# Kernel optimization log

Measured on AMD Instinct MI355X. Metric: run time of the kernel, lower is better.

Reference implementation:

```python
import jax, jax.numpy as jnp
import numpy as np
from jax import lax

A_RATIOS = (0.5, 1.0, 2.0)
A_SCALES = (8, 16, 32)
FEAT_STRIDE = 16
BASE_SIZE = 16
PRE_NMS = 6000     # n_test_pre_nms
POST_NMS = 300     # n_test_post_nms
NMS_THRESH = 0.7
MIN_SIZE = 16.0
SCALE = 1.0        # forward(scale=1.0) default
NEG = -1e10


def _anchor_base():
    # standard generate_anchor_base: centered at (8,8), ratios x scales
    py = px = BASE_SIZE / 2.0
    rows = []
    for r in A_RATIOS:
        for s in A_SCALES:
            h = BASE_SIZE * s * np.sqrt(r)
            w = BASE_SIZE * s * np.sqrt(1.0 / r)
            rows.append([py - h / 2.0, px - w / 2.0, py + h / 2.0, px + w / 2.0])
    return np.asarray(rows, np.float32)  # (A, 4)


def _all_anchors(height, width):
    base = jnp.asarray(_anchor_base())                                  # (A, 4)
    sy = (jnp.arange(height) * FEAT_STRIDE).astype(jnp.float32)
    sx = (jnp.arange(width) * FEAT_STRIDE).astype(jnp.float32)
    gy, gx = jnp.meshgrid(sy, sx, indexing='ij')
    shift = jnp.stack([gy.ravel(), gx.ravel(), gy.ravel(), gx.ravel()], axis=1)  # (K, 4)
    anch = base[None, :, :] + shift[:, None, :]                         # (K, A, 4)
    return anch.reshape(-1, 4)                                          # (K*A, 4)


def _conv(x, w, b, pad):
    y = lax.conv_general_dilated(x, w, (1, 1), [(pad, pad), (pad, pad)],
                                 dimension_numbers=('NCHW', 'OIHW', 'NCHW'))
    return y + b[None, :, None, None]


def _loc2bbox(anchors, locs):
    h = anchors[:, 2] - anchors[:, 0]
    w = anchors[:, 3] - anchors[:, 1]
    cy = anchors[:, 0] + 0.5 * h
    cx = anchors[:, 1] + 0.5 * w
    dy, dx, dh, dw = locs[:, 0], locs[:, 1], locs[:, 2], locs[:, 3]
    ncy = dy * h + cy
    ncx = dx * w + cx
    nh = jnp.exp(dh) * h
    nw = jnp.exp(dw) * w
    return jnp.stack([ncy - 0.5 * nh, ncx - 0.5 * nw,
                      ncy + 0.5 * nh, ncx + 0.5 * nw], axis=1)


def _iou_one_vs_all(box, boxes):
    ty = jnp.maximum(box[0], boxes[:, 0])
    tx = jnp.maximum(box[1], boxes[:, 1])
    by = jnp.minimum(box[2], boxes[:, 2])
    bx = jnp.minimum(box[3], boxes[:, 3])
    inter = jnp.maximum(by - ty, 0.0) * jnp.maximum(bx - tx, 0.0)
    a1 = (box[2] - box[0]) * (box[3] - box[1])
    a2 = (boxes[:, 2] - boxes[:, 0]) * (boxes[:, 3] - boxes[:, 1])
    return inter / (a1 + a2 - inter + 1e-9)


def _nms(boxes, scores):
    # greedy NMS with fixed POST_NMS output; invalid slots are zero boxes
    def step(s, _):
        i = jnp.argmax(s)
        valid = s[i] > NEG / 2
        ious = _iou_one_vs_all(boxes[i], boxes)
        s = jnp.where(ious > NMS_THRESH, NEG, s)  # suppresses self (iou=1)
        return s, (i, valid)
    _, (idx, valid) = lax.scan(step, scores, None, length=POST_NMS)
    return boxes[idx] * valid[:, None].astype(boxes.dtype)  # (POST_NMS, 4)


def _proposals(anchors, locs, fg, img_h, img_w):
    boxes = _loc2bbox(anchors, locs)
    boxes = jnp.stack([jnp.clip(boxes[:, 0], 0.0, img_h),
                       jnp.clip(boxes[:, 1], 0.0, img_w),
                       jnp.clip(boxes[:, 2], 0.0, img_h),
                       jnp.clip(boxes[:, 3], 0.0, img_w)], axis=1)
    hs = boxes[:, 2] - boxes[:, 0]
    ws = boxes[:, 3] - boxes[:, 1]
    ok = (hs >= MIN_SIZE * SCALE) & (ws >= MIN_SIZE * SCALE)
    sc = jnp.where(ok, fg, NEG)
    top_sc, idx = lax.top_k(sc, PRE_NMS)
    return _nms(boxes[idx], top_sc)


def reference(base_feat, W_conv1, b_conv1, W_score, b_score, W_loc, b_loc, img_h, img_w):
    N, _, H, W = base_feat.shape
    A = 9
    mid = jax.nn.relu(_conv(base_feat, W_conv1, b_conv1, 1))            # (N,512,H,W)
    rpn_locs = _conv(mid, W_loc, b_loc, 0).transpose(0, 2, 3, 1).reshape(N, H * W * A, 4)
    raw = _conv(mid, W_score, b_score, 0).transpose(0, 2, 3, 1)          # (N,H,W,2A)
    rpn_scores = raw.reshape(N, H * W * A, 2)
    fg = jax.nn.softmax(raw.reshape(N, H, W, A, 2), axis=-1)[..., 1].reshape(N, -1)
    anchors = _all_anchors(H, W)                                         # (H*W*A,4)
    ih, iw = float(img_h), float(img_w)
    prop = jax.vmap(lambda l, f: _proposals(anchors, l, f, ih, iw))(rpn_locs, fg)
    rois = prop.reshape(N * POST_NMS, 4)
    roi_indices = jnp.repeat(jnp.arange(N, dtype=jnp.int32), POST_NMS)
    return rpn_locs, rpn_scores, rois, roi_indices, anchors


def setup_inputs() -> dict:
    key = jax.random.key(0)
    k0, k1, k2, k3 = jax.random.split(key, 4)
    N, C, H, W = 4, 512, 64, 64
    nA = 9
    return {
        'base_feat': jax.random.normal(k0, (N, C, H, W), jnp.float32),
        'W_conv1': 0.01 * jax.random.normal(k1, (512, 512, 3, 3), jnp.float32),
        'b_conv1': jnp.zeros((512,), jnp.float32),
        'W_score': 0.01 * jax.random.normal(k2, (2 * nA, 512, 1, 1), jnp.float32),
        'b_score': jnp.zeros((2 * nA,), jnp.float32),
        'W_loc': 0.01 * jax.random.normal(k3, (4 * nA, 512, 1, 1), jnp.float32),
        'b_loc': jnp.zeros((4 * nA,), jnp.float32),
        'img_h': 1024,
        'img_w': 1024,
    }
```

## Files before the change

### kernel.cpp

```cpp
#include <hip/hip_runtime.h>
#include <math.h>

#define HH 64
#define WW 64
#define NIMG 4
#define CIN 512
#define AA 9
#define HWA (HH*WW*AA)
#define PRE_NMS 6000
#define POST_NMS 300
#define NEGV (-1e10f)
#define NEGK 0xD01502F9u
#define NWORD 94

#define OFF1 589824
#define OFF2 884736
#define OFF3 889536
#define OFF4 890736

typedef unsigned int u32;
typedef unsigned long long u64;
typedef _Float16 f16;
typedef _Float16 half8 __attribute__((ext_vector_type(8)));
typedef float f32x4 __attribute__((ext_vector_type(4)));

struct AnchBase { float v[36]; };

__device__ __forceinline__ void gload_lds16(const void* g, void* l)
{
    __builtin_amdgcn_global_load_lds((const __attribute__((address_space(1))) void*)g,
                                     (__attribute__((address_space(3))) void*)l,
                                     16, 0, 0);
}

__global__ __launch_bounds__(256) void k_prep_x(const float* __restrict__ x,
                                                f16* __restrict__ xh,
                                                f16* __restrict__ xl)
{
    __shared__ float tile[64][65];
    int ci0 = blockIdx.x * 64, y = blockIdx.y, n = blockIdx.z;
    int t = threadIdx.x;
    #pragma unroll
    for (int l = 0; l < 16; ++l) {
        int idx = l * 256 + t;
        int cc = idx >> 6, xc = idx & 63;
        tile[cc][xc] = x[((size_t)(n * CIN + ci0 + cc) * HH + y) * WW + xc];
    }
    __syncthreads();
    #pragma unroll
    for (int l = 0; l < 16; ++l) {
        int idx = l * 256 + t;
        int xc = idx >> 6, cc = idx & 63;
        float v = tile[cc][xc];
        f16 hi = (f16)v;
        f16 lo = (f16)(v - (float)hi);
        size_t o = ((size_t)(n * 64 + y) * 64 + xc) * 512 + ci0 + cc;
        xh[o] = hi; xl[o] = lo;
    }
}

__global__ __launch_bounds__(256) void k_prep_w(const float* __restrict__ W1,
                                                f16* __restrict__ wh,
                                                f16* __restrict__ wl)
{
    int idx = blockIdx.x * 256 + threadIdx.x;
    int co = idx >> 9, ci = idx & 511;
    #pragma unroll
    for (int tap = 0; tap < 9; ++tap) {
        float v = W1[(size_t)idx * 9 + tap];
        f16 hi = (f16)v;
        f16 lo = (f16)(v - (float)hi);
        size_t o = ((size_t)tap * 512 + co) * 512 + ci;
        wh[o] = hi; wl[o] = lo;
    }
}

__global__ __launch_bounds__(256, 4) void k_conv_mfma(const f16* __restrict__ xh,
                                                      const f16* __restrict__ xl,
                                                      const f16* __restrict__ wh,
                                                      const f16* __restrict__ wl,
                                                      const float* __restrict__ bias,
                                                      float* __restrict__ mid)
{
    __shared__ f16 sX[2][4][66][32];
    const int t = threadIdx.x;
    const int lid = blockIdx.x + 8 * (blockIdx.y + 32 * blockIdx.z);
    const int logical = (lid & 7) * 128 + (lid >> 3);
    const int co0 = (logical & 7) * 64;
    const int g = logical >> 3;
    const int yb = g & 31, n = g >> 5;
    const int y0 = yb * 2;
    const int wv = t >> 6, lane = t & 63;
    const int q = lane >> 4, li = lane & 15;
    const int mh = wv & 1;
    const int xhp = wv >> 1;

    {
        int pr = t >> 5, j = t & 31;
        int col = (j < 16) ? 0 : 65, e = j & 15;
        u32* p = (u32*)&sX[0][0][0][0];
        p[(pr >> 2) * 4224 + (pr & 3) * 1056 + col * 16 + e] = 0;
    }
    if (yb == 0 || yb == 31) {
        int r = (yb == 0) ? 0 : 3;
        u32* p = (u32*)&sX[0][0][0][0];
        #pragma unroll
        for (int l = 0; l < 9; ++l) {
            int idx = l * 256 + t;
            if (idx < 2112) {
                int plane = (idx >= 1056) ? 1 : 0;
                int rr = idx - plane * 1056;
                p[plane * 4224 + r * 1056 + rr] = 0;
            }
        }
    }

    f32x4 acc[2][2][2];
    #pragma unroll
    for (int mt = 0; mt < 2; ++mt)
        #pragma unroll
        for (int xn = 0; xn < 2; ++xn)
            #pragma unroll
            for (int yy = 0; yy < 2; ++yy)
                acc[mt][xn][yy] = (f32x4){0.f, 0.f, 0.f, 0.f};

    auto prefetch = [&](int ci0) {
        #pragma unroll
        for (int m = 0; m < 8; ++m) {
            int k2 = wv * 8 + m;
            int plane = k2 >> 4;
            int row = (k2 >> 2) & 3;
            int gy = y0 - 1 + row;
            if ((unsigned)gy < 64u) {
                int col = ((k2 & 3) << 4) + (lane >> 2);
                int s = (lane & 3) ^ ((lane >> 3) & 3);
                const f16* src = (plane ? xl : xh) +
                    (((size_t)(n * 64 + gy) * 64 + col) * 512 + ci0 + s * 8);
                f16* dst = &sX[0][0][0][0] + (size_t)plane * 8448 + row * 2112
                           + (1 + (k2 & 3) * 16) * 32 + lane * 8;
                gload_lds16(src, dst);
            }
        }
    };

    const size_t wb0 = (size_t)(co0 + mh * 32 + li) * 512 + q * 8;
    const f16* pWh = wh + wb0;
    const f16* pWl = wl + wb0;
    half8 wa[2][2], wn[2][2];
    auto loadW = [&](half8 (&w)[2][2], int ci0, int tap) {
        #pragma unroll
        for (int mt = 0; mt < 2; ++mt) {
            size_t off = (size_t)tap * 262144 + (size_t)mt * 8192 + ci0;
            w[0][mt] = *(const half8*)(pWh + off);
            w[1][mt] = *(const half8*)(pWl + off);
        }
    };

    const f16* pB[2][3];
    #pragma unroll
    for (int xn = 0; xn < 2; ++xn)
        #pragma unroll
        for (int kx = 0; kx < 3; ++kx) {
            int lc = xhp * 32 + xn * 16 + li + kx;
            int qe = q ^ (((lc - 1) >> 1) & 3);
            pB[xn][kx] = &sX[0][0][0][0] + lc * 32 + qe * 8;
        }

    auto loadB = [&](half8 (&Bf)[2][2][2], int tap) {
        const int ky = tap / 3, kx = tap - ky * 3;
        #pragma unroll
        for (int xn = 0; xn < 2; ++xn) {
            const f16* pb = pB[xn][kx];
            #pragma unroll
            for (int yy = 0; yy < 2; ++yy) {
                const f16* ph = pb + (yy + ky) * 2112;
                Bf[0][xn][yy] = *(const half8*)ph;
                Bf[1][xn][yy] = *(const half8*)(ph + 8448);
            }
        }
    };

    prefetch(0);
    loadW(wa, 0, 0);

    for (int chunk = 0; chunk < 16; ++chunk) {
        const int ci0 = chunk * 32;
        __syncthreads();

        half8 B0[2][2][2], Bn[2][2][2];
        loadB(B0, 0);

        #pragma unroll
        for (int tap = 0; tap < 9; ++tap) {
            if (tap < 8) {
                loadW(wn, ci0, tap + 1);
                loadB(Bn, tap + 1);
            }
            #pragma unroll
            for (int mt = 0; mt < 2; ++mt)
                #pragma unroll
                for (int xn = 0; xn < 2; ++xn)
                    #pragma unroll
                    for (int yy = 0; yy < 2; ++yy)
                        acc[mt][xn][yy] = __builtin_amdgcn_mfma_f32_16x16x32_f16(wa[0][mt], B0[0][xn][yy], acc[mt][xn][yy], 0, 0, 0);
            #pragma unroll
            for (int mt = 0; mt < 2; ++mt)
                #pragma unroll
                for (int xn = 0; xn < 2; ++xn)
                    #pragma unroll
                    for (int yy = 0; yy < 2; ++yy)
                        acc[mt][xn][yy] = __builtin_amdgcn_mfma_f32_16x16x32_f16(wa[0][mt], B0[1][xn][yy], acc[mt][xn][yy], 0, 0, 0);
            #pragma unroll
            for (int mt = 0; mt < 2; ++mt)
                #pragma unroll
                for (int xn = 0; xn < 2; ++xn)
                    #pragma unroll
                    for (int yy = 0; yy < 2; ++yy)
                        acc[mt][xn][yy] = __builtin_amdgcn_mfma_f32_16x16x32_f16(wa[1][mt], B0[0][xn][yy], acc[mt][xn][yy], 0, 0, 0);

            if (tap < 8) {
                #pragma unroll
                for (int pl = 0; pl < 2; ++pl)
                    #pragma unroll
                    for (int mt = 0; mt < 2; ++mt) wa[pl][mt] = wn[pl][mt];
                #pragma unroll
                for (int pl = 0; pl < 2; ++pl)
                    #pragma unroll
                    for (int xn = 0; xn < 2; ++xn)
                        #pragma unroll
                        for (int yy = 0; yy < 2; ++yy) B0[pl][xn][yy] = Bn[pl][xn][yy];
            }
        }

        if (chunk + 1 < 16) {
            __syncthreads();
            prefetch(ci0 + 32);
            loadW(wa, ci0 + 32, 0);
        }
    }

    #pragma unroll
    for (int mt = 0; mt < 2; ++mt) {
        #pragma unroll
        for (int r = 0; r < 4; ++r) {
            int co = co0 + mh * 32 + mt * 16 + q * 4 + r;
            float bv = bias[co];
            #pragma unroll
            for (int xn = 0; xn < 2; ++xn) {
                int xc = xhp * 32 + xn * 16 + li;
                #pragma unroll
                for (int yy = 0; yy < 2; ++yy) {
                    float v = acc[mt][xn][yy][r] + bv;
                    mid[((size_t)(n * 512 + co) * HH + y0 + yy) * WW + xc] = v > 0.f ? v : 0.f;
                }
            }
        }
    }
}

__global__ __launch_bounds__(256) void k_htrans(const float* __restrict__ Ws,
                                                const float* __restrict__ Wl,
                                                float* __restrict__ Wt2)
{
    int i = blockIdx.x * 256 + threadIdx.x;
    if (i >= 512 * 64) return;
    int ci = i >> 6, co = i & 63;
    float v = 0.f;
    if (co < 18) v = Ws[co * 512 + ci];
    else if (co < 54) v = Wl[(co - 18) * 512 + ci];
    Wt2[i] = v;
}

__global__ __launch_bounds__(256) void k_hgemm(const float* __restrict__ mid,
                                               const float* __restrict__ Wt2,
                                               float* __restrict__ sraw)
{
    __shared__ float sM[32][64];
    __shared__ float sW2[32][64];
    const int t = threadIdx.x;
    const int px0 = blockIdx.x * 64, n = blockIdx.y;
    const int tx = t & 15, ty = t >> 4;

    float acc[4][4];
    #pragma unroll
    for (int c = 0; c < 4; ++c)
        #pragma unroll
        for (int j = 0; j < 4; ++j) acc[c][j] = 0.f;

    for (int ci0 = 0; ci0 < 512; ci0 += 32) {
        __syncthreads();
        #pragma unroll
        for (int l = 0; l < 8; ++l) {
            int i = l * 256 + t;
            int ci = i >> 6, px = i & 63;
            sM[ci][px] = mid[((size_t)n * 512 + ci0 + ci) * 4096 + px0 + px];
            sW2[ci][px] = Wt2[(size_t)(ci0 + ci) * 64 + px];
        }
        __syncthreads();
        #pragma unroll
        for (int ci = 0; ci < 32; ++ci) {
            float mv[4], wv[4];
            #pragma unroll
            for (int j = 0; j < 4; ++j) mv[j] = sM[ci][tx * 4 + j];
            #pragma unroll
            for (int c = 0; c < 4; ++c) wv[c] = sW2[ci][ty * 4 + c];
            #pragma unroll
            for (int c = 0; c < 4; ++c)
                #pragma unroll
                for (int j = 0; j < 4; ++j) acc[c][j] += wv[c] * mv[j];
        }
    }
    #pragma unroll
    for (int c = 0; c < 4; ++c) {
        float4 v = make_float4(acc[c][0], acc[c][1], acc[c][2], acc[c][3]);
        *(float4*)&sraw[((size_t)n * 64 + ty * 4 + c) * 4096 + px0 + tx * 4] = v;
    }
}

__global__ __launch_bounds__(256) void k_decode(const float* __restrict__ sraw,
                                                const float* __restrict__ bsc,
                                                const float* __restrict__ blc,
                                                const int* __restrict__ ph,
                                                const int* __restrict__ pw,
                                                float* __restrict__ out,
                                                float* __restrict__ boxes,
                                                u32* __restrict__ key,
                                                AnchBase ab)
{
    int p = blockIdx.x * 256 + threadIdx.x;
    int n = p >> 12, pi = p & 4095;
    int y = pi >> 6, xq = pi & 63;

    const float* S = sraw + (size_t)n * 64 * 4096 + pi;
    float* o0 = out + (size_t)n * 147456;
    float* o1 = out + OFF1 + (size_t)n * 73728;
    float IHf = (float)(*ph), IWf = (float)(*pw);

    #pragma unroll
    for (int a = 0; a < 9; ++a) {
        float s0 = S[(size_t)(2 * a) * 4096] + bsc[2 * a];
        float s1 = S[(size_t)(2 * a + 1) * 4096] + bsc[2 * a + 1];
        float dy = S[(size_t)(18 + 4 * a) * 4096] + blc[4 * a];
        float dx = S[(size_t)(19 + 4 * a) * 4096] + blc[4 * a + 1];
        float dh = S[(size_t)(20 + 4 * a) * 4096] + blc[4 * a + 2];
        float dw = S[(size_t)(21 + 4 * a) * 4096] + blc[4 * a + 3];

        o1[(pi * 9 + a) * 2 + 0] = s0;
        o1[(pi * 9 + a) * 2 + 1] = s1;
        o0[(pi * 9 + a) * 4 + 0] = dy;
        o0[(pi * 9 + a) * 4 + 1] = dx;
        o0[(pi * 9 + a) * 4 + 2] = dh;
        o0[(pi * 9 + a) * 4 + 3] = dw;

        float mm = fmaxf(s0, s1);
        float e0 = expf(s0 - mm), e1 = expf(s1 - mm);
        float fg = e1 / (e0 + e1);

        float a0 = ab.v[4 * a + 0] + (float)(y * 16);
        float a1 = ab.v[4 * a + 1] + (float)(xq * 16);
        float a2 = ab.v[4 * a + 2] + (float)(y * 16);
        float a3 = ab.v[4 * a + 3] + (float)(xq * 16);

        float h = a2 - a0, w = a3 - a1;
        float cy = a0 + 0.5f * h, cx = a1 + 0.5f * w;
        float ncy = dy * h + cy, ncx = dx * w + cx;
        float nh = expf(dh) * h, nw = expf(dw) * w;
        float b0 = fminf(fmaxf(ncy - 0.5f * nh, 0.f), IHf);
        float b1 = fminf(fmaxf(ncx - 0.5f * nw, 0.f), IWf);
        float b2 = fminf(fmaxf(ncy + 0.5f * nh, 0.f), IHf);
        float b3 = fminf(fmaxf(ncx + 0.5f * nw, 0.f), IWf);

        bool ok = (b2 - b0 >= 16.0f) && (b3 - b1 >= 16.0f);
        float sc = ok ? fg : NEGV;

        int gi = n * HWA + pi * 9 + a;
        ((float4*)boxes)[gi] = make_float4(b0, b1, b2, b3);
        u32 u = __float_as_uint(sc);
        u32 kasc = (u & 0x80000000u) ? ~u : (u | 0x80000000u);
        key[gi] = ~kasc;
    }
}

__global__ void k_misc(float* __restrict__ out, AnchBase ab)
{
    int i = blockIdx.x * 256 + threadIdx.x;
    if (i < 4800) out[OFF2 + i] = 0.f;
    if (i < 1200) out[OFF3 + i] = (float)(i / 300);
    if (i < HWA) {
        int pi = i / 9, a = i - pi * 9;
        int y = pi >> 6, xq = pi & 63;
        out[OFF4 + i * 4 + 0] = ab.v[4 * a + 0] + (float)(y * 16);
        out[OFF4 + i * 4 + 1] = ab.v[4 * a + 1] + (float)(xq * 16);
        out[OFF4 + i * 4 + 2] = ab.v[4 * a + 2] + (float)(y * 16);
        out[OFF4 + i * 4 + 3] = ab.v[4 * a + 3] + (float)(xq * 16);
    }
}

__global__ __launch_bounds__(1024) void k_select(const u32* __restrict__ key,
                                                 u64* __restrict__ cmp,
                                                 int* __restrict__ nvalid)
{
    __shared__ int hist[256];
    __shared__ u32 sPref;
    __shared__ int sR;
    __shared__ int cLess, cEq, cVal;
    int n = blockIdx.x, t = threadIdx.x;
    const u32* k0 = key + (size_t)n * HWA;

    u32 pref = 0, mask = 0;
    int R = PRE_NMS;
    for (int pass = 0; pass < 4; ++pass) {
        int shift = 24 - pass * 8;
        if (t < 256) hist[t] = 0;
        __syncthreads();
        for (int i = t; i < HWA; i += 1024) {
            u32 k = k0[i];
            if ((k & mask) == pref) atomicAdd(&hist[(k >> shift) & 255], 1);
        }
        __syncthreads();
        if (t == 0) {
            int cum = 0;
            for (int b = 0; b < 256; ++b) {
                int c = hist[b];
                if (cum + c >= R) { sPref = pref | ((u32)b << shift); sR = R - cum; break; }
                cum += c;
            }
        }
        __syncthreads();
        pref = sPref; R = sR; mask |= (0xFFu << shift);
        __syncthreads();
    }
    u32 T = pref;
    if (t == 0) { cLess = 0; cEq = 0; cVal = 0; }
    __syncthreads();
    for (int i = t; i < HWA; i += 1024) {
        u32 k = k0[i];
        if (k < NEGK) atomicAdd(&cVal, 1);
        if (k < T) {
            int p = atomicAdd(&cLess, 1);
            cmp[(size_t)n * 8192 + p] = ((u64)k << 32) | (u32)i;
        } else if (k == T) {
            int p = atomicAdd(&cEq, 1);
            if (p < R) cmp[(size_t)n * 8192 + (PRE_NMS - 1 - p)] = ((u64)k << 32) | (u32)i;
        }
    }
    for (int i = PRE_NMS + t; i < 8192; i += 1024) cmp[(size_t)n * 8192 + i] = ~0ull;
    __syncthreads();
    if (t == 0) nvalid[n] = cVal < PRE_NMS ? cVal : PRE_NMS;
}

__global__ __launch_bounds__(1024) void k_sort(const u64* __restrict__ cmp,
                                               const float* __restrict__ boxes,
                                               float* __restrict__ boxesS)
{
    __shared__ u64 sK[8192];
    int n = blockIdx.x, t = threadIdx.x;
    for (int i = t; i < 8192; i += 1024) sK[i] = cmp[(size_t)n * 8192 + i];
    for (unsigned k = 2; k <= 8192; k <<= 1) {
        for (unsigned j = k >> 1; j > 0; j >>= 1) {
            __syncthreads();
            #pragma unroll
            for (int v = 0; v < 8; ++v) {
                int i = v * 1024 + t;
                int ixj = i ^ (int)j;
                if (ixj > i) {
                    u64 a = sK[i], b = sK[ixj];
                    bool up = ((i & (int)k) == 0);
                    if (up ? (a > b) : (a < b)) { sK[i] = b; sK[ixj] = a; }
                }
            }
        }
    }
    __syncthreads();
    const float4* bsrc = (const float4*)boxes + (size_t)n * HWA;
    float4* bdst = (float4*)boxesS + (size_t)n * PRE_NMS;
    for (int i = t; i < PRE_NMS; i += 1024) {
        u32 idx = (u32)(sK[i] & 0xFFFFFFFFu);
        bdst[i] = bsrc[idx];
    }
}

__global__ __launch_bounds__(64) void k_iou(const float* __restrict__ boxesS,
                                            u64* __restrict__ mask)
{
    __shared__ float4 cb[64];
    int w = blockIdx.x, ic = blockIdx.y, n = blockIdx.z;
    if (w < ic) return;
    int t = threadIdx.x;
    const float4* B = (const float4*)boxesS + (size_t)n * PRE_NMS;
    int jc = w * 64 + t;
    cb[t] = (jc < PRE_NMS) ? B[jc] : make_float4(0.f, 0.f, 0.f, 0.f);
    __syncthreads();
    int i = ic * 64 + t;
    if (i >= PRE_NMS) return;
    float4 bb = B[i];
    float area1 = (bb.z - bb.x) * (bb.w - bb.y);
    u64 m = 0;
    #pragma unroll 8
    for (int j = 0; j < 64; ++j) {
        float4 o = cb[j];
        float ty_ = fmaxf(bb.x, o.x), tx_ = fmaxf(bb.y, o.y);
        float by_ = fminf(bb.z, o.z), bx_ = fminf(bb.w, o.w);
        float inter = fmaxf(by_ - ty_, 0.f) * fmaxf(bx_ - tx_, 0.f);
        float area2 = (o.z - o.x) * (o.w - o.y);
        float iou = inter / (area1 + area2 - inter + 1e-9f);
        if (iou > 0.7f) m |= (1ull << j);
    }
    mask[((size_t)n * PRE_NMS + i) * NWORD + w] = m;
}

__global__ __launch_bounds__(64) void k_nms3(const u64* __restrict__ mask,
                                             const int* __restrict__ nvalid,
                                             const float* __restrict__ boxesS,
                                             float* __restrict__ rois)
{
    int n = blockIdx.x, lane = threadIdx.x;
    int nv = nvalid[n];
    const u64* M = mask + (size_t)n * PRE_NMS * NWORD;
    const float4* B = (const float4*)boxesS + (size_t)n * PRE_NMS;

    auto vmask = [&](int w) -> u64 {
        int lo = w * 64;
        if (nv >= lo + 64) return ~0ull;
        if (nv <= lo) return 0ull;
        return (1ull << (nv - lo)) - 1ull;
    };
    u64 vm0 = vmask(lane);
    u64 vm1 = (lane < NWORD - 64) ? vmask(64 + lane) : 0ull;
    u64 rem0 = 0, rem1 = 0;

    int cnt = 0;
    while (cnt < POST_NMS) {
        u64 c0 = (~rem0) & vm0;
        u64 c1 = (~rem1) & vm1;
        int sel;
        u64 b0 = __ballot(c0 != 0);
        if (b0) {
            int l = __builtin_ctzll(b0);
            u64 w = __shfl(c0, l);
            sel = l * 64 + __builtin_ctzll(w);
        } else {
            u64 b1 = __ballot(c1 != 0);
            if (!b1) break;
            int l = __builtin_ctzll(b1);
            u64 w = __shfl(c1, l);
            sel = (64 + l) * 64 + __builtin_ctzll(w);
        }
        if (lane == 0) {
            float4 bb = B[sel];
            float* orow = rois + (size_t)(n * POST_NMS + cnt) * 4;
            orow[0] = bb.x; orow[1] = bb.y; orow[2] = bb.z; orow[3] = bb.w;
        }
        const u64* Mr = M + (size_t)sel * NWORD;
        rem0 |= Mr[lane];
        if (lane < NWORD - 64) rem1 |= Mr[64 + lane];
        cnt++;
    }
}

extern "C" void kernel_launch(void* const* d_in, const int* in_sizes, int n_in,
                              void* d_out, int out_size, void* d_ws, size_t ws_size,
                              hipStream_t stream)
{
    const float* x  = (const float*)d_in[0];
    const float* W1 = (const float*)d_in[1];
    const float* b1 = (const float*)d_in[2];
    const float* Ws = (const float*)d_in[3];
    const float* bs = (const float*)d_in[4];
    const float* Wl = (const float*)d_in[5];
    const float* bl = (const float*)d_in[6];
    const int* ih   = (const int*)d_in[7];
    const int* iw   = (const int*)d_in[8];
    float* out = (float*)d_out;
    char* ws = (char*)d_ws;

    f16*   Wh2    = (f16*)  (ws);
    f16*   Wl2    = (f16*)  (ws + 4718592);
    float* mid    = (float*)(ws + 9437184);
    f16*   xh     = (f16*)  (ws + 42991616);
    f16*   xl     = (f16*)  (ws + 59768832);
    float* boxes  = (float*)(ws + 42991616);
    u32*   key    = (u32*)  (ws + 45350912);
    u64*   cmp    = (u64*)  (ws + 45940736);
    float* boxesS = (float*)(ws + 46202880);
    int*   nval   = (int*)  (ws + 46586880);
    float* Wt2    = (float*)(ws);
    float* sraw   = (float*)(ws + 262144);
    u64*   iomask = (u64*)  (ws + 9437184);

    AnchBase ab;
    for (int a = 0; a < 9; ++a) {
        int ri = a / 3, si = a - ri * 3;
        double s = (double)(8 << si);
        double rr = (ri == 0) ? 0.5 : ((ri == 1) ? 1.0 : 2.0);
        double hh = 16.0 * s * sqrt(rr);
        double wd = 16.0 * s * sqrt(1.0 / rr);
        ab.v[a * 4 + 0] = (float)(8.0 - hh * 0.5);
        ab.v[a * 4 + 1] = (float)(8.0 - wd * 0.5);
        ab.v[a * 4 + 2] = (float)(8.0 + hh * 0.5);
        ab.v[a * 4 + 3] = (float)(8.0 + wd * 0.5);
    }

    k_prep_x<<<dim3(8, 64, 4), 256, 0, stream>>>(x, xh, xl);
    k_prep_w<<<1024, 256, 0, stream>>>(W1, Wh2, Wl2);
    k_conv_mfma<<<dim3(8, 32, 4), 256, 0, stream>>>(xh, xl, Wh2, Wl2, b1, mid);
    k_htrans<<<128, 256, 0, stream>>>(Ws, Wl, Wt2);
    k_hgemm<<<dim3(64, 4), 256, 0, stream>>>(mid, Wt2, sraw);
    k_decode<<<64, 256, 0, stream>>>(sraw, bs, bl, ih, iw, out, boxes, key, ab);
    k_misc<<<144, 256, 0, stream>>>(out, ab);
    k_select<<<4, 1024, 0, stream>>>(key, cmp, nval);
    k_sort<<<4, 1024, 0, stream>>>(cmp, boxes, boxesS);
    k_iou<<<dim3(NWORD, NWORD, NIMG), 64, 0, stream>>>(boxesS, iomask);
    k_nms3<<<NIMG, 64, 0, stream>>>(iomask, nval, boxesS, out + OFF2);
}
```

Baseline: 826.3 us.

## Fuse small kernels and speculate next pick in greedy NMS loop

Drops the weight transpose kernel: the head GEMM now reads the score and loc weights directly while filling shared memory. The misc output writes (zeros, roi indices, anchors) move into the decode kernel. Candidate selection and bitonic sort are merged into one kernel that keeps keys in shared memory instead of a global round trip. The serial NMS loop prefetches the suppression row of the next likely candidate so two boxes can sometimes be accepted per iteration. Together these cut launch count and shorten the latency-bound NMS chain, at the cost of strided, uncoalesced weight loads in the GEMM.

```diff
diff --git a/kernel.cpp b/kernel.cpp
--- a/kernel.cpp
+++ b/kernel.cpp
@@ -258,21 +258,9 @@
     }
 }
 
-__global__ __launch_bounds__(256) void k_htrans(const float* __restrict__ Ws,
-                                                const float* __restrict__ Wl,
-                                                float* __restrict__ Wt2)
-{
-    int i = blockIdx.x * 256 + threadIdx.x;
-    if (i >= 512 * 64) return;
-    int ci = i >> 6, co = i & 63;
-    float v = 0.f;
-    if (co < 18) v = Ws[co * 512 + ci];
-    else if (co < 54) v = Wl[(co - 18) * 512 + ci];
-    Wt2[i] = v;
-}
-
 __global__ __launch_bounds__(256) void k_hgemm(const float* __restrict__ mid,
-                                               const float* __restrict__ Wt2,
+                                               const float* __restrict__ Ws,
+                                               const float* __restrict__ Wls,
                                                float* __restrict__ sraw)
 {
     __shared__ float sM[32][64];
@@ -294,7 +282,11 @@
             int i = l * 256 + t;
             int ci = i >> 6, px = i & 63;
             sM[ci][px] = mid[((size_t)n * 512 + ci0 + ci) * 4096 + px0 + px];
-            sW2[ci][px] = Wt2[(size_t)(ci0 + ci) * 64 + px];
+            int co = px;
+            float v = 0.f;
+            if (co < 18) v = Ws[co * 512 + ci0 + ci];
+            else if (co < 54) v = Wls[(co - 18) * 512 + ci0 + ci];
+            sW2[ci][px] = v;
         }
         __syncthreads();
         #pragma unroll
@@ -331,6 +323,9 @@
     int n = p >> 12, pi = p & 4095;
     int y = pi >> 6, xq = pi & 63;
 
+    if (p < 4800) out[OFF2 + p] = 0.f;
+    else if (p < 6000) out[OFF3 + (p - 4800)] = (float)((p - 4800) / 300);
+
     const float* S = sraw + (size_t)n * 64 * 4096 + pi;
     float* o0 = out + (size_t)n * 147456;
     float* o1 = out + OFF1 + (size_t)n * 73728;
@@ -360,6 +355,11 @@
         float a1 = ab.v[4 * a + 1] + (float)(xq * 16);
         float a2 = ab.v[4 * a + 2] + (float)(y * 16);
         float a3 = ab.v[4 * a + 3] + (float)(xq * 16);
+
+        if (n == 0) {
+            float* oa = out + OFF4 + (size_t)(pi * 9 + a) * 4;
+            oa[0] = a0; oa[1] = a1; oa[2] = a2; oa[3] = a3;
+        }
 
         float h = a2 - a0, w = a3 - a1;
         float cy = a0 + 0.5f * h, cx = a1 + 0.5f * w;
@@ -381,25 +381,12 @@
     }
 }
 
-__global__ void k_misc(float* __restrict__ out, AnchBase ab)
-{
-    int i = blockIdx.x * 256 + threadIdx.x;
-    if (i < 4800) out[OFF2 + i] = 0.f;
-    if (i < 1200) out[OFF3 + i] = (float)(i / 300);
-    if (i < HWA) {
-        int pi = i / 9, a = i - pi * 9;
-        int y = pi >> 6, xq = pi & 63;
-        out[OFF4 + i * 4 + 0] = ab.v[4 * a + 0] + (float)(y * 16);
-        out[OFF4 + i * 4 + 1] = ab.v[4 * a + 1] + (float)(xq * 16);
-        out[OFF4 + i * 4 + 2] = ab.v[4 * a + 2] + (float)(y * 16);
-        out[OFF4 + i * 4 + 3] = ab.v[4 * a + 3] + (float)(xq * 16);
-    }
-}
-
-__global__ __launch_bounds__(1024) void k_select(const u32* __restrict__ key,
-                                                 u64* __restrict__ cmp,
-                                                 int* __restrict__ nvalid)
-{
+__global__ __launch_bounds__(1024) void k_selsort(const u32* __restrict__ key,
+                                                  const float* __restrict__ boxes,
+                                                  float* __restrict__ boxesS,
+                                                  int* __restrict__ nvalid)
+{
+    __shared__ u64 sK[8192];
     __shared__ int hist[256];
     __shared__ u32 sPref;
     __shared__ int sR;
@@ -438,24 +425,16 @@
         if (k < NEGK) atomicAdd(&cVal, 1);
         if (k < T) {
             int p = atomicAdd(&cLess, 1);
-            cmp[(size_t)n * 8192 + p] = ((u64)k << 32) | (u32)i;
+            sK[p] = ((u64)k << 32) | (u32)i;
         } else if (k == T) {
             int p = atomicAdd(&cEq, 1);
-            if (p < R) cmp[(size_t)n * 8192 + (PRE_NMS - 1 - p)] = ((u64)k << 32) | (u32)i;
-        }
-    }
-    for (int i = PRE_NMS + t; i < 8192; i += 1024) cmp[(size_t)n * 8192 + i] = ~0ull;
+            if (p < R) sK[PRE_NMS - 1 - p] = ((u64)k << 32) | (u32)i;
+        }
+    }
+    for (int i = PRE_NMS + t; i < 8192; i += 1024) sK[i] = ~0ull;
     __syncthreads();
     if (t == 0) nvalid[n] = cVal < PRE_NMS ? cVal : PRE_NMS;
-}
-
-__global__ __launch_bounds__(1024) void k_sort(const u64* __restrict__ cmp,
-                                               const float* __restrict__ boxes,
-                                               float* __restrict__ boxesS)
-{
-    __shared__ u64 sK[8192];
-    int n = blockIdx.x, t = threadIdx.x;
-    for (int i = t; i < 8192; i += 1024) sK[i] = cmp[(size_t)n * 8192 + i];
+
     for (unsigned k = 2; k <= 8192; k <<= 1) {
         for (unsigned j = k >> 1; j > 0; j >>= 1) {
             __syncthreads();
@@ -525,36 +504,62 @@
         if (nv <= lo) return 0ull;
         return (1ull << (nv - lo)) - 1ull;
     };
-    u64 vm0 = vmask(lane);
-    u64 vm1 = (lane < NWORD - 64) ? vmask(64 + lane) : 0ull;
-    u64 rem0 = 0, rem1 = 0;
-
-    int cnt = 0;
-    while (cnt < POST_NMS) {
-        u64 c0 = (~rem0) & vm0;
-        u64 c1 = (~rem1) & vm1;
-        int sel;
-        u64 b0 = __ballot(c0 != 0);
+    u64 c0 = vmask(lane);
+    u64 c1 = (lane < NWORD - 64) ? vmask(64 + lane) : 0ull;
+
+    auto firstbit = [&](u64 a0, u64 a1) -> int {
+        u64 b0 = __ballot(a0 != 0);
         if (b0) {
             int l = __builtin_ctzll(b0);
-            u64 w = __shfl(c0, l);
-            sel = l * 64 + __builtin_ctzll(w);
-        } else {
-            u64 b1 = __ballot(c1 != 0);
-            if (!b1) break;
-            int l = __builtin_ctzll(b1);
-            u64 w = __shfl(c1, l);
-            sel = (64 + l) * 64 + __builtin_ctzll(w);
-        }
+            u64 w = __shfl(a0, l);
+            return l * 64 + __builtin_ctzll(w);
+        }
+        u64 b1 = __ballot(a1 != 0);
+        if (!b1) return -1;
+        int l = __builtin_ctzll(b1);
+        u64 w = __shfl(a1, l);
+        return (64 + l) * 64 + __builtin_ctzll(w);
+    };
+    auto clearbit = [&](u64& a0, u64& a1, int s) {
+        int ws = s >> 6, b = s & 63;
+        if (lane == ws) a0 &= ~(1ull << b);
+        if (lane + 64 == ws) a1 &= ~(1ull << b);
+    };
+    auto emit = [&](int s, int c) {
         if (lane == 0) {
-            float4 bb = B[sel];
-            float* orow = rois + (size_t)(n * POST_NMS + cnt) * 4;
+            float4 bb = B[s];
+            float* orow = rois + (size_t)(n * POST_NMS + c) * 4;
             orow[0] = bb.x; orow[1] = bb.y; orow[2] = bb.z; orow[3] = bb.w;
         }
+    };
+
+    int cnt = 0;
+    int sel = firstbit(c0, c1);
+    while (sel >= 0 && cnt < POST_NMS) {
         const u64* Mr = M + (size_t)sel * NWORD;
-        rem0 |= Mr[lane];
-        if (lane < NWORD - 64) rem1 |= Mr[64 + lane];
-        cnt++;
+        u64 m0 = Mr[lane];
+        u64 m1 = (lane < NWORD - 64) ? Mr[64 + lane] : 0ull;
+
+        u64 d0 = c0, d1 = c1;
+        clearbit(d0, d1, sel);
+        int pred = firstbit(d0, d1);
+        u64 p0 = 0, p1 = 0;
+        if (pred >= 0) {
+            const u64* Pr = M + (size_t)pred * NWORD;
+            p0 = Pr[lane];
+            p1 = (lane < NWORD - 64) ? Pr[64 + lane] : 0ull;
+        }
+
+        emit(sel, cnt); cnt++;
+        c0 = d0 & ~m0; c1 = d1 & ~m1;
+        int nxt = firstbit(c0, c1);
+        if (nxt >= 0 && nxt == pred && cnt < POST_NMS) {
+            emit(pred, cnt); cnt++;
+            clearbit(c0, c1, pred);
+            c0 &= ~p0; c1 &= ~p1;
+            nxt = firstbit(c0, c1);
+        }
+        sel = nxt;
     }
 }
 
@@ -581,10 +586,8 @@
     f16*   xl     = (f16*)  (ws + 59768832);
     float* boxes  = (float*)(ws + 42991616);
     u32*   key    = (u32*)  (ws + 45350912);
-    u64*   cmp    = (u64*)  (ws + 45940736);
     float* boxesS = (float*)(ws + 46202880);
     int*   nval   = (int*)  (ws + 46586880);
-    float* Wt2    = (float*)(ws);
     float* sraw   = (float*)(ws + 262144);
     u64*   iomask = (u64*)  (ws + 9437184);
 
@@ -604,12 +607,9 @@
     k_prep_x<<<dim3(8, 64, 4), 256, 0, stream>>>(x, xh, xl);
     k_prep_w<<<1024, 256, 0, stream>>>(W1, Wh2, Wl2);
     k_conv_mfma<<<dim3(8, 32, 4), 256, 0, stream>>>(xh, xl, Wh2, Wl2, b1, mid);
-    k_htrans<<<128, 256, 0, stream>>>(Ws, Wl, Wt2);
-    k_hgemm<<<dim3(64, 4), 256, 0, stream>>>(mid, Wt2, sraw);
+    k_hgemm<<<dim3(64, 4), 256, 0, stream>>>(mid, Ws, Wl, sraw);
     k_decode<<<64, 256, 0, stream>>>(sraw, bs, bl, ih, iw, out, boxes, key, ab);
-    k_misc<<<144, 256, 0, stream>>>(out, ab);
-    k_select<<<4, 1024, 0, stream>>>(key, cmp, nval);
-    k_sort<<<4, 1024, 0, stream>>>(cmp, boxes, boxesS);
+    k_selsort<<<4, 1024, 0, stream>>>(key, boxes, boxesS, nval);
     k_iou<<<dim3(NWORD, NWORD, NIMG), 64, 0, stream>>>(boxesS, iomask);
     k_nms3<<<NIMG, 64, 0, stream>>>(iomask, nval, boxesS, out + OFF2);
 }
```

Measured after the change: 896.7 us. 1.09x slower.
